# Optimization experiments

Measured on AMD Instinct MI355X. Metric: run time of the kernel, lower is better.

## Reference

```python
import jax, jax.numpy as jnp
import numpy as np
import math

H = 8  # num_heads

def setup_inputs() -> dict:
    key = jax.random.key(0)
    ks = jax.random.split(key, 12)
    B, N, M, k = 2, 8192, 8192, 32
    dq, dk, dv = 256, 256, 256
    s = 1.0 / math.sqrt(dq)
    inp = {
        'Q': jax.random.normal(ks[0], (B, N, dq), dtype=jnp.float32),
        'K': jax.random.normal(ks[1], (B, M, dk), dtype=jnp.float32),
        'neighbours': jax.random.randint(ks[2], (B, N, k), 0, M),
        'Wq': jax.random.normal(ks[3], (dq, dv), dtype=jnp.float32) * s,
        'bq': jnp.zeros((dv,), dtype=jnp.float32),
        'Wk': jax.random.normal(ks[4], (dk, dv), dtype=jnp.float32) * s,
        'bk': jnp.zeros((dv,), dtype=jnp.float32),
        'Wv': jax.random.normal(ks[5], (dk, dv), dtype=jnp.float32) * s,
        'bv': jnp.zeros((dv,), dtype=jnp.float32),
        'Wo': jax.random.normal(ks[6], (dv, dv), dtype=jnp.float32) * (1.0 / math.sqrt(dv)),
        'bo': jnp.zeros((dv,), dtype=jnp.float32),
    }
    return inp

def reference(Q, K, neighbours, Wq, bq, Wk, bk, Wv, bv, Wo, bo):
    B, N, _ = Q.shape
    dv = Wq.shape[1]
    ds = dv // H
    # project and split heads (contiguous channel chunks == reshape)
    Qh = (Q @ Wq + bq).reshape(B, N, H, ds)            # [B,N,H,ds]
    Kh = (K @ Wk + bk).reshape(B, -1, H, ds)           # [B,M,H,ds]
    Vh = (K @ Wv + bv).reshape(B, -1, H, ds)           # [B,M,H,ds]
    # gather per-node kNN neighbour keys/values: [B,N,k,H,ds]
    gather = jax.vmap(lambda x, idx: x[idx])
    Kn = gather(Kh, neighbours)
    Vn = gather(Vh, neighbours)
    # scale uses full latent size (faithful to original), not head dim
    scale = 1.0 / math.sqrt(dv)
    E = jnp.einsum('bnhd,bnkhd->bnhk', Qh, Kn) * scale  # [B,N,H,k]
    A = jax.nn.softmax(E, axis=-1)
    AV = jnp.einsum('bnhk,bnkhd->bnhd', A, Vn).reshape(B, N, dv)
    return AV @ Wo + bo
```

## Files before the change

### kernel.cpp

```cpp
#include <hip/hip_runtime.h>
#include <hip/hip_bf16.h>
#include <stdint.h>

typedef unsigned short u16;
typedef __attribute__((ext_vector_type(8))) short short8;
typedef __attribute__((ext_vector_type(4))) float f32x4;

__device__ __forceinline__ u16 f2bf(float f) {
    union { float f; unsigned int i; } v; v.f = f;
    unsigned int b = v.i;
    return (u16)((b + 0x7FFFu + ((b >> 16) & 1u)) >> 16);
}

__device__ __forceinline__ short8 cvt8(float4 a, float4 b) {
    union { __hip_bfloat162 h[4]; short8 s; } u;
    u.h[0] = __float22bfloat162_rn(make_float2(a.x, a.y));
    u.h[1] = __float22bfloat162_rn(make_float2(a.z, a.w));
    u.h[2] = __float22bfloat162_rn(make_float2(b.x, b.y));
    u.h[3] = __float22bfloat162_rn(make_float2(b.z, b.w));
    return u.s;
}

typedef const __attribute__((address_space(1))) void* as1cv;
typedef __attribute__((address_space(3))) void* as3v;
__device__ __forceinline__ void gload16(const void* g, void* l) {
    __builtin_amdgcn_global_load_lds((as1cv)g, (as3v)l, 16, 0, 0);
}

__device__ __forceinline__ void up2(unsigned int v, float& lo, float& hi) {
    union { unsigned int i; float f; } a, b;
    a.i = v << 16; b.i = v & 0xffff0000u;
    lo = a.f; hi = b.f;
}

__global__ __launch_bounds__(256) void wprep(
    const float* __restrict__ W0, const float* __restrict__ W1,
    const float* __restrict__ W2, const float* __restrict__ W3,
    u16* __restrict__ T0, u16* __restrict__ T1,
    u16* __restrict__ T2, u16* __restrict__ T3)
{
    const float* W = blockIdx.z == 0 ? W0 : blockIdx.z == 1 ? W1 : blockIdx.z == 2 ? W2 : W3;
    u16*        T  = blockIdx.z == 0 ? T0 : blockIdx.z == 1 ? T1 : blockIdx.z == 2 ? T2 : T3;
    __shared__ u16 ts[64][65];
    int k0 = blockIdx.x * 64, n0 = blockIdx.y * 64;
    int t = threadIdx.x;
    int r = t >> 2, cq = (t & 3) * 16;
    const float4* src = reinterpret_cast<const float4*>(W + (k0 + r) * 256 + n0 + cq);
    for (int u = 0; u < 4; ++u) {
        float4 v = src[u];
        int c = cq + u * 4;
        ts[r][c + 0] = f2bf(v.x); ts[r][c + 1] = f2bf(v.y);
        ts[r][c + 2] = f2bf(v.z); ts[r][c + 3] = f2bf(v.w);
    }
    __syncthreads();
    u16* dst = T + (n0 + r) * 256 + k0 + cq;
    for (int u = 0; u < 16; ++u) dst[u] = ts[cq + u][r];
}

__global__ __launch_bounds__(256) void gemm_proj(
    const float* __restrict__ Q, const float* __restrict__ K,
    const u16* __restrict__ Wtq, const u16* __restrict__ Wtk, const u16* __restrict__ Wtv,
    const float* __restrict__ bq, const float* __restrict__ bk, const float* __restrict__ bv,
    u16* __restrict__ Qh, u16* __restrict__ Kh, u16* __restrict__ Vh)
{
    int z = blockIdx.z;
    const float* Af   = (z == 0) ? Q   : K;
    const u16*   Wt   = (z == 0) ? Wtq : (z == 1) ? Wtk : Wtv;
    const float* bias = (z == 0) ? bq  : (z == 1) ? bk  : bv;
    u16*         C    = (z == 0) ? Qh  : (z == 1) ? Kh  : Vh;

    __shared__ float Asf[128 * 64];
    __shared__ u16   Bs[128 * 64];

    int t = threadIdx.x;
    int lane = t & 63, w = t >> 6;
    int row0 = blockIdx.x * 128, col0 = blockIdx.y * 128;
    int wr = (w >> 1) * 64, wc = (w & 1) * 64;
    int qd = lane >> 4, md = lane & 15;

    f32x4 acc[4][4] = {};

    for (int kt = 0; kt < 256; kt += 64) {
#pragma unroll
        for (int u = 0; u < 8; ++u) {
            int chunk = w * 8 + u;
            int s = chunk * 64 + lane;
            int r = s >> 4, c = s & 15;
            gload16(Af + (size_t)(row0 + r) * 256 + kt + ((c ^ (r & 15)) * 4),
                    (char*)Asf + chunk * 1024);
        }
#pragma unroll
        for (int u = 0; u < 4; ++u) {
            int chunk = w * 4 + u;
            int s = chunk * 64 + lane;
            int r = s >> 3, c = s & 7;
            gload16(Wt + (size_t)(col0 + r) * 256 + kt + ((c ^ (r & 7)) * 8),
                    (char*)Bs + chunk * 1024);
        }
        __syncthreads();
#pragma unroll
        for (int ks = 0; ks < 64; ks += 32) {
            short8 af[4], bf[4];
#pragma unroll
            for (int i = 0; i < 4; ++i) {
                int ar = wr + i * 16 + md;
                int c0 = (ks >> 2) + qd * 2;
                int x = ar & 15;
                float4 fa0 = reinterpret_cast<const float4*>(Asf)[ar * 16 + (c0 ^ x)];
                float4 fa1 = reinterpret_cast<const float4*>(Asf)[ar * 16 + ((c0 + 1) ^ x)];
                af[i] = cvt8(fa0, fa1);
            }
#pragma unroll
            for (int j = 0; j < 4; ++j) {
                int br = wc + j * 16 + md;
                int slot = ((ks >> 3) + qd) ^ (br & 7);
                bf[j] = reinterpret_cast<const short8*>(Bs)[br * 8 + slot];
            }
#pragma unroll
            for (int i = 0; i < 4; ++i)
#pragma unroll
                for (int j = 0; j < 4; ++j)
                    acc[i][j] = __builtin_amdgcn_mfma_f32_16x16x32_bf16(
                        af[i], bf[j], acc[i][j], 0, 0, 0);
        }
        __syncthreads();
    }

#pragma unroll
    for (int i = 0; i < 4; ++i)
#pragma unroll
        for (int j = 0; j < 4; ++j) {
            int col = col0 + wc + j * 16 + md;
            float b = bias[col];
#pragma unroll
            for (int r = 0; r < 4; ++r) {
                int row = row0 + wr + i * 16 + qd * 4 + r;
                C[(size_t)row * 256 + col] = f2bf(acc[i][j][r] + b);
            }
        }
}

__global__ __launch_bounds__(256) void gemm_out(
    const u16* __restrict__ Ab, const u16* __restrict__ Wt,
    const float* __restrict__ bias, float* __restrict__ Cout)
{
    __shared__ u16 As[64 * 64];
    __shared__ u16 Bs[128 * 64];

    int t = threadIdx.x;
    int lane = t & 63, w = t >> 6;
    int row0 = blockIdx.x * 64, col0 = blockIdx.y * 128;
    int wr = (w >> 1) * 32, wc = (w & 1) * 64;
    int qd = lane >> 4, md = lane & 15;

    f32x4 acc[2][4] = {};

    for (int kt = 0; kt < 256; kt += 64) {
#pragma unroll
        for (int u = 0; u < 2; ++u) {
            int chunk = w * 2 + u;
            int s = chunk * 64 + lane;
            int r = s >> 3, c = s & 7;
            gload16(Ab + (size_t)(row0 + r) * 256 + kt + ((c ^ (r & 7)) * 8),
                    (char*)As + chunk * 1024);
        }
#pragma unroll
        for (int u = 0; u < 4; ++u) {
            int chunk = w * 4 + u;
            int s = chunk * 64 + lane;
            int r = s >> 3, c = s & 7;
            gload16(Wt + (size_t)(col0 + r) * 256 + kt + ((c ^ (r & 7)) * 8),
                    (char*)Bs + chunk * 1024);
        }
        __syncthreads();
#pragma unroll
        for (int ks = 0; ks < 64; ks += 32) {
            short8 af[2], bf[4];
#pragma unroll
            for (int i = 0; i < 2; ++i) {
                int ar = wr + i * 16 + md;
                int slot = ((ks >> 3) + qd) ^ (ar & 7);
                af[i] = reinterpret_cast<const short8*>(As)[ar * 8 + slot];
            }
#pragma unroll
            for (int j = 0; j < 4; ++j) {
                int br = wc + j * 16 + md;
                int slot = ((ks >> 3) + qd) ^ (br & 7);
                bf[j] = reinterpret_cast<const short8*>(Bs)[br * 8 + slot];
            }
#pragma unroll
            for (int i = 0; i < 2; ++i)
#pragma unroll
                for (int j = 0; j < 4; ++j)
                    acc[i][j] = __builtin_amdgcn_mfma_f32_16x16x32_bf16(
                        af[i], bf[j], acc[i][j], 0, 0, 0);
        }
        __syncthreads();
    }

#pragma unroll
    for (int i = 0; i < 2; ++i)
#pragma unroll
        for (int j = 0; j < 4; ++j) {
            int col = col0 + wc + j * 16 + md;
            float b = bias[col];
#pragma unroll
            for (int r = 0; r < 4; ++r) {
                int row = row0 + wr + i * 16 + qd * 4 + r;
                Cout[(size_t)row * 256 + col] = acc[i][j][r] + b;
            }
        }
}

__global__ __launch_bounds__(256) void attn(
    const u16* __restrict__ Qh, const u16* __restrict__ Kh, const u16* __restrict__ Vh,
    const int* __restrict__ nbr, u16* __restrict__ AVb)
{
    __shared__ int jbs[4][32];

    int t = threadIdx.x;
    int w = t >> 6, lane = t & 63;
    int row = blockIdx.x * 4 + w;
    int b = row >> 13;
    int bbase = b << 13;

    int c8 = lane & 31;
    int jh = lane >> 5;

    if (lane < 32) {
        int ji = nbr[(size_t)row * 32 + lane];
        jbs[w][lane] = (bbase + ji) * 256;
    }

    float qf[8];
    {
        uint4 qw = *reinterpret_cast<const uint4*>(Qh + (size_t)row * 256 + c8 * 8);
        up2(qw.x, qf[0], qf[1]); up2(qw.y, qf[2], qf[3]);
        up2(qw.z, qf[4], qf[5]); up2(qw.w, qf[6], qf[7]);
    }

    float e16[16];
#pragma unroll
    for (int jj = 0; jj < 16; ++jj) {
        int koff = jbs[w][jh * 16 + jj];
        uint4 kw = *reinterpret_cast<const uint4*>(Kh + (size_t)koff + c8 * 8);
        float k0, k1;
        float p = 0.f;
        up2(kw.x, k0, k1); p = fmaf(qf[0], k0, p); p = fmaf(qf[1], k1, p);
        up2(kw.y, k0, k1); p = fmaf(qf[2], k0, p); p = fmaf(qf[3], k1, p);
        up2(kw.z, k0, k1); p = fmaf(qf[4], k0, p); p = fmaf(qf[5], k1, p);
        up2(kw.w, k0, k1); p = fmaf(qf[6], k0, p); p = fmaf(qf[7], k1, p);
        p += __shfl_xor(p, 1);
        p += __shfl_xor(p, 2);
        e16[jj] = p * 0.0625f;
    }

    float m = e16[0];
#pragma unroll
    for (int jj = 1; jj < 16; ++jj) m = fmaxf(m, e16[jj]);
    m = fmaxf(m, __shfl_xor(m, 32));
    float s = 0.f;
#pragma unroll
    for (int jj = 0; jj < 16; ++jj) { e16[jj] = __expf(e16[jj] - m); s += e16[jj]; }
    s += __shfl_xor(s, 32);
    float rs = 1.0f / s;
#pragma unroll
    for (int jj = 0; jj < 16; ++jj) e16[jj] *= rs;

    float acc[8] = {};
#pragma unroll
    for (int jj = 0; jj < 16; ++jj) {
        int voff = jbs[w][jh * 16 + jj];
        uint4 vv = *reinterpret_cast<const uint4*>(Vh + (size_t)voff + c8 * 8);
        float v0, v1;
        float wgt = e16[jj];
        up2(vv.x, v0, v1); acc[0] = fmaf(wgt, v0, acc[0]); acc[1] = fmaf(wgt, v1, acc[1]);
        up2(vv.y, v0, v1); acc[2] = fmaf(wgt, v0, acc[2]); acc[3] = fmaf(wgt, v1, acc[3]);
        up2(vv.z, v0, v1); acc[4] = fmaf(wgt, v0, acc[4]); acc[5] = fmaf(wgt, v1, acc[5]);
        up2(vv.w, v0, v1); acc[6] = fmaf(wgt, v0, acc[6]); acc[7] = fmaf(wgt, v1, acc[7]);
    }
#pragma unroll
    for (int u = 0; u < 8; ++u) acc[u] += __shfl_xor(acc[u], 32);

    if (lane < 32) {
        union { __hip_bfloat162 h[4]; uint4 u4; } o;
        o.h[0] = __float22bfloat162_rn(make_float2(acc[0], acc[1]));
        o.h[1] = __float22bfloat162_rn(make_float2(acc[2], acc[3]));
        o.h[2] = __float22bfloat162_rn(make_float2(acc[4], acc[5]));
        o.h[3] = __float22bfloat162_rn(make_float2(acc[6], acc[7]));
        *reinterpret_cast<uint4*>(AVb + (size_t)row * 256 + c8 * 8) = o.u4;
    }
}

extern "C" void kernel_launch(void* const* d_in, const int* in_sizes, int n_in,
                              void* d_out, int out_size, void* d_ws, size_t ws_size,
                              hipStream_t stream) {
    const float* Q   = (const float*)d_in[0];
    const float* K   = (const float*)d_in[1];
    const int*   nbr = (const int*)d_in[2];
    const float* Wq  = (const float*)d_in[3];
    const float* bq  = (const float*)d_in[4];
    const float* Wk  = (const float*)d_in[5];
    const float* bk  = (const float*)d_in[6];
    const float* Wv  = (const float*)d_in[7];
    const float* bv  = (const float*)d_in[8];
    const float* Wo  = (const float*)d_in[9];
    const float* bo  = (const float*)d_in[10];
    float* out = (float*)d_out;

    char* ws = (char*)d_ws;
    size_t off = 0;
    auto alloc = [&](size_t bytes) -> void* {
        void* p = ws + off;
        off += (bytes + 255) & ~(size_t)255;
        return p;
    };
    const size_t MN = 16384;
    u16* Wtq = (u16*)alloc(256 * 256 * 2);
    u16* Wtk = (u16*)alloc(256 * 256 * 2);
    u16* Wtv = (u16*)alloc(256 * 256 * 2);
    u16* Wto = (u16*)alloc(256 * 256 * 2);
    u16* Qh  = (u16*)alloc(MN * 256 * 2);
    u16* Kh  = (u16*)alloc(MN * 256 * 2);
    u16* Vh  = (u16*)alloc(MN * 256 * 2);
    u16* AVb = (u16*)alloc(MN * 256 * 2);

    wprep<<<dim3(4, 4, 4), 256, 0, stream>>>(Wq, Wk, Wv, Wo, Wtq, Wtk, Wtv, Wto);
    gemm_proj<<<dim3(128, 2, 3), 256, 0, stream>>>(Q, K, Wtq, Wtk, Wtv,
                                                   bq, bk, bv, Qh, Kh, Vh);
    attn<<<dim3(4096), 256, 0, stream>>>(Qh, Kh, Vh, nbr, AVb);
    gemm_out<<<dim3(256, 2), 256, 0, stream>>>(AVb, Wto, bo, out);
}
```

Before: 161.5 us.

## Fuse K/V projections sharing A tile and prefetch gathered K/V rows in attention

```diff
diff --git a/kernel.cpp b/kernel.cpp
--- a/kernel.cpp
+++ b/kernel.cpp
@@ -63,31 +63,113 @@
     const float* __restrict__ bq, const float* __restrict__ bk, const float* __restrict__ bv,
     u16* __restrict__ Qh, u16* __restrict__ Kh, u16* __restrict__ Vh)
 {
-    int z = blockIdx.z;
-    const float* Af   = (z == 0) ? Q   : K;
-    const u16*   Wt   = (z == 0) ? Wtq : (z == 1) ? Wtk : Wtv;
-    const float* bias = (z == 0) ? bq  : (z == 1) ? bk  : bv;
-    u16*         C    = (z == 0) ? Qh  : (z == 1) ? Kh  : Vh;
-
-    __shared__ float Asf[128 * 64];
-    __shared__ u16   Bs[128 * 64];
+    int z = blockIdx.y;
+    const float* Af  = z ? K   : Q;
+    const u16*   Wt0 = z ? Wtk : Wtq;
+    const float* bi0 = z ? bk  : bq;
+    u16*         C0  = z ? Kh  : Qh;
+
+    __shared__ float Asf[32 * 64];
+    __shared__ u16   B0s[256 * 64];
+    __shared__ u16   B1s[256 * 64];
 
     int t = threadIdx.x;
     int lane = t & 63, w = t >> 6;
-    int row0 = blockIdx.x * 128, col0 = blockIdx.y * 128;
-    int wr = (w >> 1) * 64, wc = (w & 1) * 64;
+    int row0 = blockIdx.x * 32;
+    int rowgrp = (w >> 1) * 16, colh = (w & 1) * 128;
     int qd = lane >> 4, md = lane & 15;
 
-    f32x4 acc[4][4] = {};
+    f32x4 acc0[8] = {};
+    f32x4 acc1[8] = {};
 
     for (int kt = 0; kt < 256; kt += 64) {
 #pragma unroll
-        for (int u = 0; u < 8; ++u) {
-            int chunk = w * 8 + u;
+        for (int u = 0; u < 2; ++u) {
+            int chunk = w * 2 + u;
             int s = chunk * 64 + lane;
             int r = s >> 4, c = s & 15;
             gload16(Af + (size_t)(row0 + r) * 256 + kt + ((c ^ (r & 15)) * 4),
                     (char*)Asf + chunk * 1024);
+        }
+#pragma unroll
+        for (int u = 0; u < 8; ++u) {
+            int chunk = w * 8 + u;
+            int s = chunk * 64 + lane;
+            int r = s >> 3, c = s & 7;
+            gload16(Wt0 + (size_t)r * 256 + kt + ((c ^ (r & 7)) * 8),
+                    (char*)B0s + chunk * 1024);
+        }
+        if (z) {
+#pragma unroll
+            for (int u = 0; u < 8; ++u) {
+                int chunk = w * 8 + u;
+                int s = chunk * 64 + lane;
+                int r = s >> 3, c = s & 7;
+                gload16(Wtv + (size_t)r * 256 + kt + ((c ^ (r & 7)) * 8),
+                        (char*)B1s + chunk * 1024);
+            }
+        }
+        __syncthreads();
+#pragma unroll
+        for (int ks = 0; ks < 64; ks += 32) {
+            int ar = rowgrp + md;
+            int c0 = (ks >> 2) + qd * 2;
+            int x = ar & 15;
+            float4 fa0 = reinterpret_cast<const float4*>(Asf)[ar * 16 + (c0 ^ x)];
+            float4 fa1 = reinterpret_cast<const float4*>(Asf)[ar * 16 + ((c0 + 1) ^ x)];
+            short8 af = cvt8(fa0, fa1);
+#pragma unroll
+            for (int j = 0; j < 8; ++j) {
+                int br = colh + j * 16 + md;
+                int slot = ((ks >> 3) + qd) ^ (br & 7);
+                short8 bf0 = reinterpret_cast<const short8*>(B0s)[br * 8 + slot];
+                acc0[j] = __builtin_amdgcn_mfma_f32_16x16x32_bf16(af, bf0, acc0[j], 0, 0, 0);
+                if (z) {
+                    short8 bf1 = reinterpret_cast<const short8*>(B1s)[br * 8 + slot];
+                    acc1[j] = __builtin_amdgcn_mfma_f32_16x16x32_bf16(af, bf1, acc1[j], 0, 0, 0);
+                }
+            }
+        }
+        __syncthreads();
+    }
+
+#pragma unroll
+    for (int j = 0; j < 8; ++j) {
+        int col = colh + j * 16 + md;
+        float b0 = bi0[col];
+        float b1 = z ? bv[col] : 0.f;
+#pragma unroll
+        for (int r = 0; r < 4; ++r) {
+            int row = row0 + rowgrp + qd * 4 + r;
+            C0[(size_t)row * 256 + col] = f2bf(acc0[j][r] + b0);
+            if (z) Vh[(size_t)row * 256 + col] = f2bf(acc1[j][r] + b1);
+        }
+    }
+}
+
+__global__ __launch_bounds__(256) void gemm_out(
+    const u16* __restrict__ Ab, const u16* __restrict__ Wt,
+    const float* __restrict__ bias, float* __restrict__ Cout)
+{
+    __shared__ u16 As[64 * 64];
+    __shared__ u16 Bs[128 * 64];
+
+    int t = threadIdx.x;
+    int lane = t & 63, w = t >> 6;
+    int row0 = blockIdx.x * 64, col0 = blockIdx.y * 128;
+    int wr = (w >> 1) * 32, wc = (w & 1) * 64;
+    int qd = lane >> 4, md = lane & 15;
+
+    f32x4 acc[2][4] = {};
+
+    for (int kt = 0; kt < 256; kt += 64) {
+#pragma unroll
+        for (int u = 0; u < 2; ++u) {
+            int chunk = w * 2 + u;
+            int s = chunk * 64 + lane;
+            int r = s >> 3, c = s & 7;
+            gload16(Ab + (size_t)(row0 + r) * 256 + kt + ((c ^ (r & 7)) * 8),
+                    (char*)As + chunk * 1024);
         }
 #pragma unroll
         for (int u = 0; u < 4; ++u) {
@@ -100,81 +182,6 @@
         __syncthreads();
 #pragma unroll
         for (int ks = 0; ks < 64; ks += 32) {
-            short8 af[4], bf[4];
-#pragma unroll
-            for (int i = 0; i < 4; ++i) {
-                int ar = wr + i * 16 + md;
-                int c0 = (ks >> 2) + qd * 2;
-                int x = ar & 15;
-                float4 fa0 = reinterpret_cast<const float4*>(Asf)[ar * 16 + (c0 ^ x)];
-                float4 fa1 = reinterpret_cast<const float4*>(Asf)[ar * 16 + ((c0 + 1) ^ x)];
-                af[i] = cvt8(fa0, fa1);
-            }
-#pragma unroll
-            for (int j = 0; j < 4; ++j) {
-                int br = wc + j * 16 + md;
-                int slot = ((ks >> 3) + qd) ^ (br & 7);
-                bf[j] = reinterpret_cast<const short8*>(Bs)[br * 8 + slot];
-            }
-#pragma unroll
-            for (int i = 0; i < 4; ++i)
-#pragma unroll
-                for (int j = 0; j < 4; ++j)
-                    acc[i][j] = __builtin_amdgcn_mfma_f32_16x16x32_bf16(
-                        af[i], bf[j], acc[i][j], 0, 0, 0);
-        }
-        __syncthreads();
-    }
-
-#pragma unroll
-    for (int i = 0; i < 4; ++i)
-#pragma unroll
-        for (int j = 0; j < 4; ++j) {
-            int col = col0 + wc + j * 16 + md;
-            float b = bias[col];
-#pragma unroll
-            for (int r = 0; r < 4; ++r) {
-                int row = row0 + wr + i * 16 + qd * 4 + r;
-                C[(size_t)row * 256 + col] = f2bf(acc[i][j][r] + b);
-            }
-        }
-}
-
-__global__ __launch_bounds__(256) void gemm_out(
-    const u16* __restrict__ Ab, const u16* __restrict__ Wt,
-    const float* __restrict__ bias, float* __restrict__ Cout)
-{
-    __shared__ u16 As[64 * 64];
-    __shared__ u16 Bs[128 * 64];
-
-    int t = threadIdx.x;
-    int lane = t & 63, w = t >> 6;
-    int row0 = blockIdx.x * 64, col0 = blockIdx.y * 128;
-    int wr = (w >> 1) * 32, wc = (w & 1) * 64;
-    int qd = lane >> 4, md = lane & 15;
-
-    f32x4 acc[2][4] = {};
-
-    for (int kt = 0; kt < 256; kt += 64) {
-#pragma unroll
-        for (int u = 0; u < 2; ++u) {
-            int chunk = w * 2 + u;
-            int s = chunk * 64 + lane;
-            int r = s >> 3, c = s & 7;
-            gload16(Ab + (size_t)(row0 + r) * 256 + kt + ((c ^ (r & 7)) * 8),
-                    (char*)As + chunk * 1024);
-        }
-#pragma unroll
-        for (int u = 0; u < 4; ++u) {
-            int chunk = w * 4 + u;
-            int s = chunk * 64 + lane;
-            int r = s >> 3, c = s & 7;
-            gload16(Wt + (size_t)(col0 + r) * 256 + kt + ((c ^ (r & 7)) * 8),
-                    (char*)Bs + chunk * 1024);
-        }
-        __syncthreads();
-#pragma unroll
-        for (int ks = 0; ks < 64; ks += 32) {
             short8 af[2], bf[4];
 #pragma unroll
             for (int i = 0; i < 2; ++i) {
@@ -239,17 +246,27 @@
         up2(qw.z, qf[4], qf[5]); up2(qw.w, qf[6], qf[7]);
     }
 
+    uint4 kw[16], vv[16];
+#pragma unroll
+    for (int jj = 0; jj < 16; ++jj) {
+        int off = jbs[w][jh * 16 + jj];
+        kw[jj] = *reinterpret_cast<const uint4*>(Kh + (size_t)off + c8 * 8);
+    }
+#pragma unroll
+    for (int jj = 0; jj < 16; ++jj) {
+        int off = jbs[w][jh * 16 + jj];
+        vv[jj] = *reinterpret_cast<const uint4*>(Vh + (size_t)off + c8 * 8);
+    }
+
     float e16[16];
 #pragma unroll
     for (int jj = 0; jj < 16; ++jj) {
-        int koff = jbs[w][jh * 16 + jj];
-        uint4 kw = *reinterpret_cast<const uint4*>(Kh + (size_t)koff + c8 * 8);
         float k0, k1;
         float p = 0.f;
-        up2(kw.x, k0, k1); p = fmaf(qf[0], k0, p); p = fmaf(qf[1], k1, p);
-        up2(kw.y, k0, k1); p = fmaf(qf[2], k0, p); p = fmaf(qf[3], k1, p);
-        up2(kw.z, k0, k1); p = fmaf(qf[4], k0, p); p = fmaf(qf[5], k1, p);
-        up2(kw.w, k0, k1); p = fmaf(qf[6], k0, p); p = fmaf(qf[7], k1, p);
+        up2(kw[jj].x, k0, k1); p = fmaf(qf[0], k0, p); p = fmaf(qf[1], k1, p);
+        up2(kw[jj].y, k0, k1); p = fmaf(qf[2], k0, p); p = fmaf(qf[3], k1, p);
+        up2(kw[jj].z, k0, k1); p = fmaf(qf[4], k0, p); p = fmaf(qf[5], k1, p);
+        up2(kw[jj].w, k0, k1); p = fmaf(qf[6], k0, p); p = fmaf(qf[7], k1, p);
         p += __shfl_xor(p, 1);
         p += __shfl_xor(p, 2);
         e16[jj] = p * 0.0625f;
@@ -270,14 +287,12 @@
     float acc[8] = {};
 #pragma unroll
     for (int jj = 0; jj < 16; ++jj) {
-        int voff = jbs[w][jh * 16 + jj];
-        uint4 vv = *reinterpret_cast<const uint4*>(Vh + (size_t)voff + c8 * 8);
         float v0, v1;
         float wgt = e16[jj];
-        up2(vv.x, v0, v1); acc[0] = fmaf(wgt, v0, acc[0]); acc[1] = fmaf(wgt, v1, acc[1]);
-        up2(vv.y, v0, v1); acc[2] = fmaf(wgt, v0, acc[2]); acc[3] = fmaf(wgt, v1, acc[3]);
-        up2(vv.z, v0, v1); acc[4] = fmaf(wgt, v0, acc[4]); acc[5] = fmaf(wgt, v1, acc[5]);
-        up2(vv.w, v0, v1); acc[6] = fmaf(wgt, v0, acc[6]); acc[7] = fmaf(wgt, v1, acc[7]);
+        up2(vv[jj].x, v0, v1); acc[0] = fmaf(wgt, v0, acc[0]); acc[1] = fmaf(wgt, v1, acc[1]);
+        up2(vv[jj].y, v0, v1); acc[2] = fmaf(wgt, v0, acc[2]); acc[3] = fmaf(wgt, v1, acc[3]);
+        up2(vv[jj].z, v0, v1); acc[4] = fmaf(wgt, v0, acc[4]); acc[5] = fmaf(wgt, v1, acc[5]);
+        up2(vv[jj].w, v0, v1); acc[6] = fmaf(wgt, v0, acc[6]); acc[7] = fmaf(wgt, v1, acc[7]);
     }
 #pragma unroll
     for (int u = 0; u < 8; ++u) acc[u] += __shfl_xor(acc[u], 32);
@@ -326,8 +341,8 @@
     u16* AVb = (u16*)alloc(MN * 256 * 2);
 
     wprep<<<dim3(4, 4, 4), 256, 0, stream>>>(Wq, Wk, Wv, Wo, Wtq, Wtk, Wtv, Wto);
-    gemm_proj<<<dim3(128, 2, 3), 256, 0, stream>>>(Q, K, Wtq, Wtk, Wtv,
-                                                   bq, bk, bv, Qh, Kh, Vh);
+    gemm_proj<<<dim3(512, 2), 256, 0, stream>>>(Q, K, Wtq, Wtk, Wtv,
+                                                bq, bk, bv, Qh, Kh, Vh);
     attn<<<dim3(4096), 256, 0, stream>>>(Qh, Kh, Vh, nbr, AVb);
     gemm_out<<<dim3(256, 2), 256, 0, stream>>>(AVb, Wto, bo, out);
 }
```

Measured after the change: 170.2 us. 5.4% more time.
